# Optimization experiments

Measured on AMD Instinct MI355X. Metric: run time of the kernel, lower is better.

## Reference

```python
import jax, jax.numpy as jnp
import numpy as np

D_MODEL, D_INNER, D_STATE, DT_RANK, D_CONV = 768, 1536, 16, 48, 4
B, L = 2, 2048


def setup_inputs() -> dict:
    key = jax.random.key(0)
    ks = jax.random.split(key, 8)
    s = 0.02
    return {
        "x": jax.random.normal(ks[0], (B, L, D_MODEL), jnp.float32),
        "norm_w": jnp.ones((D_MODEL,), jnp.float32),
        "in_proj_w": jax.random.normal(ks[1], (2 * D_INNER, D_MODEL), jnp.float32) * s,
        "conv_w": jax.random.normal(ks[2], (D_INNER, 1, D_CONV), jnp.float32) * s,
        "conv_b": jnp.zeros((D_INNER,), jnp.float32),
        "x_proj_w": jax.random.normal(ks[3], (DT_RANK + 2 * D_STATE, D_INNER), jnp.float32) * s,
        "dt_proj_w": jax.random.normal(ks[4], (D_INNER, DT_RANK), jnp.float32) * s,
        "dt_proj_b": jax.random.normal(ks[5], (D_INNER,), jnp.float32) * s,
        "A_log": jnp.broadcast_to(jnp.log(jnp.arange(1, D_STATE + 1, dtype=jnp.float32)), (D_INNER, D_STATE)).copy(),
        "D": jnp.ones((D_INNER,), jnp.float32),
        "out_proj_w": jax.random.normal(ks[6], (D_MODEL, D_INNER), jnp.float32) * s,
    }


def _mamba_block(x, norm_w, in_proj_w, conv_w, conv_b, x_proj_w,
                 dt_proj_w, dt_proj_b, A_log, D, out_proj_w):
    residual = x
    # RMSNorm
    h = x * jax.lax.rsqrt(jnp.mean(x * x, axis=-1, keepdims=True) + 1e-5) * norm_w
    # in_proj -> chunk into (hs, gate)
    xz = jnp.einsum('bld,ed->ble', h, in_proj_w)          # [B,L,2*Di]
    xh, z = jnp.split(xz, 2, axis=-1)                     # each [B,L,Di]
    # causal depthwise conv1d (kernel D_CONV) + SiLU
    xt = jnp.transpose(xh, (0, 2, 1))                     # [B,Di,L]
    xt = jnp.pad(xt, ((0, 0), (0, 0), (D_CONV - 1, 0)))
    xc = jax.lax.conv_general_dilated(xt, conv_w, (1,), 'VALID',
                                      feature_group_count=D_INNER)
    xc = jax.nn.silu(xc + conv_b[None, :, None])
    xc = jnp.transpose(xc, (0, 2, 1))                     # [B,L,Di]
    # x_proj -> (dt, B, C)
    proj = jnp.einsum('bld,ed->ble', xc, x_proj_w)        # [B,L,dt_rank+2N]
    dt, Bm, Cm = jnp.split(proj, [DT_RANK, DT_RANK + D_STATE], axis=-1)
    delta = jax.nn.softplus(jnp.einsum('blr,dr->bld', dt, dt_proj_w) + dt_proj_b)  # [B,L,Di]
    A = -jnp.exp(A_log)                                   # [Di,N]
    dA = jnp.exp(delta[..., None] * A)                    # [B,L,Di,N]
    dBx = delta[..., None] * Bm[:, :, None, :] * xc[..., None]  # [B,L,Di,N]
    # selective scan over the sequence axis
    def step(hst, inp):
        dA_t, dBx_t, C_t = inp                            # [B,Di,N],[B,Di,N],[B,N]
        hst = dA_t * hst + dBx_t
        y = jnp.einsum('bdn,bn->bd', hst, C_t)
        return hst, y
    h0 = jnp.zeros((x.shape[0], D_INNER, D_STATE), x.dtype)
    _, ys = jax.lax.scan(step, h0, (jnp.moveaxis(dA, 1, 0),
                                    jnp.moveaxis(dBx, 1, 0),
                                    jnp.moveaxis(Cm, 1, 0)))
    y = jnp.moveaxis(ys, 0, 1)                            # [B,L,Di]
    y = y + xc * D                                        # skip connection D
    y = y * jax.nn.silu(z)                                # gate
    out = jnp.einsum('bld,ed->ble', y, out_proj_w)        # [B,L,Dm]
    return residual + out, residual


def reference(x, norm_w, in_proj_w, conv_w, conv_b, x_proj_w,
              dt_proj_w, dt_proj_b, A_log, D, out_proj_w):
    return _mamba_block(x, norm_w, in_proj_w, conv_w, conv_b, x_proj_w,
                        dt_proj_w, dt_proj_b, A_log, D, out_proj_w)
```

## Files before the change

### kernel.cpp

```cpp
#include <hip/hip_runtime.h>
#include <cstdint>
#include <cstddef>

typedef __bf16 bf16_t;
typedef __bf16 bf16x8 __attribute__((ext_vector_type(8)));
typedef float  f32x4  __attribute__((ext_vector_type(4)));

#define D_MODEL 768
#define D_INNER 1536
#define D_STATE 16
#define DT_RANK 48
#define NB      2
#define SEQ     2048
#define NTOK    (NB*SEQ)
#define XPROJ_N (DT_RANK + 2*D_STATE)
#define LC      32
#define NCHUNK  (SEQ/LC)
#define XP_KS   4
#define XP_KC   (D_INNER/XP_KS)

#define N_INW (2*D_INNER*D_MODEL)
#define N_XPW (XPROJ_N*D_INNER)
#define N_DTW (D_INNER*DT_RANK)
#define N_OPW (D_MODEL*D_INNER)
#define N_CVT (N_INW+N_XPW+N_DTW+N_OPW)
#define CVT_BLOCKS (N_CVT/1024)

typedef __attribute__((address_space(1))) void gvoid_t;
typedef __attribute__((address_space(3))) void lvoid_t;
__device__ __forceinline__ void g2lds16(const bf16_t* g, bf16_t* l) {
    __builtin_amdgcn_global_load_lds((gvoid_t*)g, (lvoid_t*)l, 16, 0, 0);
}

__global__ __launch_bounds__(256)
void prep_kernel(const float* __restrict__ in_proj_w, bf16_t* __restrict__ w_in,
                 const float* __restrict__ x_proj_w,  bf16_t* __restrict__ w_xp,
                 const float* __restrict__ dt_proj_w, bf16_t* __restrict__ w_dt,
                 const float* __restrict__ out_proj_w,bf16_t* __restrict__ w_op,
                 const float* __restrict__ x, const float* __restrict__ norm_w,
                 bf16_t* __restrict__ h, float* __restrict__ proj,
                 float* __restrict__ out0, float* __restrict__ out1) {
    const int blk = blockIdx.x;
    const int tid = threadIdx.x;
    if (blk < CVT_BLOCKS) {
        int off = (blk * 256 + tid) * 4;
        const float* s; bf16_t* d;
        if (off < N_INW) { s = in_proj_w + off; d = w_in + off; }
        else if ((off -= N_INW) < N_XPW) { s = x_proj_w + off; d = w_xp + off; }
        else if ((off -= N_XPW) < N_DTW) { s = dt_proj_w + off; d = w_dt + off; }
        else { off -= N_DTW; s = out_proj_w + off; d = w_op + off; }
        float4 v = *(const float4*)s;
        d[0] = (bf16_t)v.x; d[1] = (bf16_t)v.y;
        d[2] = (bf16_t)v.z; d[3] = (bf16_t)v.w;
        return;
    }
    int t = blk - CVT_BLOCKS;
    if (tid < XPROJ_N) proj[(size_t)t * XPROJ_N + tid] = 0.f;
    const float* xr = x + (size_t)t * D_MODEL;
    float v[3];
    float ss = 0.f;
#pragma unroll
    for (int i = 0; i < 3; i++) { v[i] = xr[tid + 256*i]; ss += v[i]*v[i]; }
#pragma unroll
    for (int off = 32; off >= 1; off >>= 1) ss += __shfl_down(ss, off);
    __shared__ float red[4];
    int lane = tid & 63, wv = tid >> 6;
    if (lane == 0) red[wv] = ss;
    __syncthreads();
    float tot = red[0] + red[1] + red[2] + red[3];
    float r = rsqrtf(tot * (1.f/(float)D_MODEL) + 1e-5f);
#pragma unroll
    for (int i = 0; i < 3; i++) {
        size_t idx = (size_t)t*D_MODEL + tid + 256*i;
        h[idx] = (bf16_t)(v[i] * r * norm_w[tid + 256*i]);
        out0[idx] = v[i];
        out1[idx] = v[i];
    }
}

__global__ __launch_bounds__(256)
void gemm_nt128(const bf16_t* __restrict__ A, int lda,
                const bf16_t* __restrict__ B, int ldb,
                bf16_t* __restrict__ C, int ldc, int K) {
    __shared__ __align__(16) bf16_t As[2][128*32];
    __shared__ __align__(16) bf16_t Bs[2][128*32];
    const int tid = threadIdx.x;
    const int wave = tid >> 6, lane = tid & 63;
    const int quad = lane >> 4, l16 = lane & 15;
    const int nbx = gridDim.x, nby = gridDim.y;
    int bid = blockIdx.y * nbx + blockIdx.x;
    const int cpx = (nbx * nby) >> 3;
    bid = (bid & 7) * cpx + (bid >> 3);
    const int m0 = (bid / nby) * 128, n0 = (bid % nby) * 128;
    const int wr = (wave >> 1) * 64, wc = (wave & 1) * 64;

    const int s0 = tid, s1 = tid + 256;
    const int r0 = s0 >> 2, q0 = ((s0 & 3) ^ ((r0 >> 1) & 3)) << 3;
    const int r1 = s1 >> 2, q1 = ((s1 & 3) ^ ((r1 >> 1) & 3)) << 3;

    const bf16_t* Ar0 = A + (size_t)(m0 + r0)*lda + q0;
    const bf16_t* Ar1 = A + (size_t)(m0 + r1)*lda + q1;
    const bf16_t* Br0 = B + (size_t)(n0 + r0)*ldb + q0;
    const bf16_t* Br1 = B + (size_t)(n0 + r1)*ldb + q1;

    f32x4 acc[4][4] = {};
    const int nit = K >> 5;

    g2lds16(Ar0, &As[0][wave*512]);
    g2lds16(Ar1, &As[0][wave*512 + 2048]);
    g2lds16(Br0, &Bs[0][wave*512]);
    g2lds16(Br1, &Bs[0][wave*512 + 2048]);

    for (int it = 0; it < nit; it++) {
        __syncthreads();
        if (it + 1 < nit) {
            int k = (it + 1) << 5;
            int nb = (it + 1) & 1;
            g2lds16(Ar0 + k, &As[nb][wave*512]);
            g2lds16(Ar1 + k, &As[nb][wave*512 + 2048]);
            g2lds16(Br0 + k, &Bs[nb][wave*512]);
            g2lds16(Br1 + k, &Bs[nb][wave*512 + 2048]);
        }
        const int buf = it & 1;
        bf16x8 af[4], bfr[4];
#pragma unroll
        for (int i = 0; i < 4; i++) {
            int rr = wr + i*16 + l16;
            af[i] = *(const bf16x8*)&As[buf][rr*32 + ((quad ^ ((rr >> 1) & 3)) << 3)];
        }
#pragma unroll
        for (int j = 0; j < 4; j++) {
            int rr = wc + j*16 + l16;
            bfr[j] = *(const bf16x8*)&Bs[buf][rr*32 + ((quad ^ ((rr >> 1) & 3)) << 3)];
        }
#pragma unroll
        for (int i = 0; i < 4; i++)
#pragma unroll
            for (int j = 0; j < 4; j++)
                acc[i][j] = __builtin_amdgcn_mfma_f32_16x16x32_bf16(af[i], bfr[j], acc[i][j], 0, 0, 0);
    }

#pragma unroll
    for (int i = 0; i < 4; i++)
#pragma unroll
        for (int j = 0; j < 4; j++) {
            int n = n0 + wc + j*16 + l16;
#pragma unroll
            for (int rr = 0; rr < 4; rr++) {
                int m = m0 + wr + i*16 + quad*4 + rr;
                C[(size_t)m * ldc + n] = (bf16_t)acc[i][j][rr];
            }
        }
}

__global__ __launch_bounds__(256)
void gemm_op(const bf16_t* __restrict__ A, const bf16_t* __restrict__ B,
             float* __restrict__ C) {
    __shared__ __align__(16) bf16_t As[2][128*32];
    __shared__ __align__(16) bf16_t Bs[2][128*32];
    const int tid = threadIdx.x;
    const int wave = tid >> 6, lane = tid & 63;
    const int quad = lane >> 4, l16 = lane & 15;
    const int nbx = gridDim.x, nby = gridDim.y;
    int bid = blockIdx.y * nbx + blockIdx.x;
    const int cpx = (nbx * nby) >> 3;
    bid = (bid & 7) * cpx + (bid >> 3);
    const int m0 = (bid / nby) * 128, n0 = (bid % nby) * 128;
    const int kbase = blockIdx.z * (D_INNER/2);
    const int wr = (wave >> 1) * 64, wc = (wave & 1) * 64;

    const int s0 = tid, s1 = tid + 256;
    const int r0 = s0 >> 2, q0 = ((s0 & 3) ^ ((r0 >> 1) & 3)) << 3;
    const int r1 = s1 >> 2, q1 = ((s1 & 3) ^ ((r1 >> 1) & 3)) << 3;

    const bf16_t* Ar0 = A + (size_t)(m0 + r0)*D_INNER + kbase + q0;
    const bf16_t* Ar1 = A + (size_t)(m0 + r1)*D_INNER + kbase + q1;
    const bf16_t* Br0 = B + (size_t)(n0 + r0)*D_INNER + kbase + q0;
    const bf16_t* Br1 = B + (size_t)(n0 + r1)*D_INNER + kbase + q1;

    f32x4 acc[4][4] = {};
    const int nit = (D_INNER/2) >> 5;

    g2lds16(Ar0, &As[0][wave*512]);
    g2lds16(Ar1, &As[0][wave*512 + 2048]);
    g2lds16(Br0, &Bs[0][wave*512]);
    g2lds16(Br1, &Bs[0][wave*512 + 2048]);

    for (int it = 0; it < nit; it++) {
        __syncthreads();
        if (it + 1 < nit) {
            int k = (it + 1) << 5;
            int nb = (it + 1) & 1;
            g2lds16(Ar0 + k, &As[nb][wave*512]);
            g2lds16(Ar1 + k, &As[nb][wave*512 + 2048]);
            g2lds16(Br0 + k, &Bs[nb][wave*512]);
            g2lds16(Br1 + k, &Bs[nb][wave*512 + 2048]);
        }
        const int buf = it & 1;
        bf16x8 af[4], bfr[4];
#pragma unroll
        for (int i = 0; i < 4; i++) {
            int rr = wr + i*16 + l16;
            af[i] = *(const bf16x8*)&As[buf][rr*32 + ((quad ^ ((rr >> 1) & 3)) << 3)];
        }
#pragma unroll
        for (int j = 0; j < 4; j++) {
            int rr = wc + j*16 + l16;
            bfr[j] = *(const bf16x8*)&Bs[buf][rr*32 + ((quad ^ ((rr >> 1) & 3)) << 3)];
        }
#pragma unroll
        for (int i = 0; i < 4; i++)
#pragma unroll
            for (int j = 0; j < 4; j++)
                acc[i][j] = __builtin_amdgcn_mfma_f32_16x16x32_bf16(af[i], bfr[j], acc[i][j], 0, 0, 0);
    }

#pragma unroll
    for (int i = 0; i < 4; i++)
#pragma unroll
        for (int j = 0; j < 4; j++) {
            int n = n0 + wc + j*16 + l16;
#pragma unroll
            for (int rr = 0; rr < 4; rr++) {
                int m = m0 + wr + i*16 + quad*4 + rr;
                unsafeAtomicAdd(&C[(size_t)m * D_MODEL + n], acc[i][j][rr]);
            }
        }
}

__global__ __launch_bounds__(256)
void gemm_xp(const bf16_t* __restrict__ A, const bf16_t* __restrict__ B,
             float* __restrict__ proj) {
    __shared__ __align__(16) bf16_t As[64*32];
    __shared__ __align__(16) bf16_t Bs[64*32];
    const int tid = threadIdx.x;
    const int m0 = blockIdx.x * 64, n0 = blockIdx.y * 64, kbase = blockIdx.z * XP_KC;
    const int r  = tid >> 2, p8 = (tid & 3) << 3;
    const int q8 = (((tid & 3) ^ ((r >> 1) & 3)) << 3);
    const int wave = tid >> 6, lane = tid & 63;
    const int quad = lane >> 4, l16 = lane & 15;

    f32x4 acc[4] = {{0.f,0.f,0.f,0.f},{0.f,0.f,0.f,0.f},
                    {0.f,0.f,0.f,0.f},{0.f,0.f,0.f,0.f}};

    for (int k0 = 0; k0 < XP_KC; k0 += 32) {
        int gk = kbase + k0 + q8;
        uint4 va = *(const uint4*)(A + (size_t)(m0 + r) * D_INNER + gk);
        *(uint4*)&As[r*32 + p8] = va;
        uint4 vb = {0u,0u,0u,0u};
        int nr = n0 + r;
        if (nr < XPROJ_N)
            vb = *(const uint4*)(B + (size_t)nr * D_INNER + gk);
        *(uint4*)&Bs[r*32 + p8] = vb;

        __syncthreads();
        int ra = wave*16 + l16;
        bf16x8 af = *(const bf16x8*)&As[ra*32 + ((quad ^ ((ra >> 1) & 3)) << 3)];
#pragma unroll
        for (int nt = 0; nt < 4; nt++) {
            int rb = nt*16 + l16;
            bf16x8 bfg = *(const bf16x8*)&Bs[rb*32 + ((quad ^ ((rb >> 1) & 3)) << 3)];
            acc[nt] = __builtin_amdgcn_mfma_f32_16x16x32_bf16(af, bfg, acc[nt], 0, 0, 0);
        }
        __syncthreads();
    }

#pragma unroll
    for (int nt = 0; nt < 4; nt++) {
        int n = n0 + nt*16 + l16;
        if (n >= XPROJ_N) continue;
#pragma unroll
        for (int rr = 0; rr < 4; rr++) {
            int m = m0 + wave*16 + quad*4 + rr;
            unsafeAtomicAdd(&proj[(size_t)m * XPROJ_N + n], acc[nt][rr]);
        }
    }
}

__global__ __launch_bounds__(192)
void conv_silu_kernel(const bf16_t* __restrict__ xz,
                      const float* __restrict__ cw,
                      const float* __restrict__ cb,
                      bf16_t* __restrict__ xc) {
    const int t0 = blockIdx.x * 8;
    const int l0 = t0 & (SEQ - 1);
    const int d = threadIdx.x * 8;

    float cwf[32];
#pragma unroll
    for (int q = 0; q < 8; q++)
        *(float4*)&cwf[q*4] = *(const float4*)&cw[d*4 + q*4];

    float cbv[8];
    *(float4*)&cbv[0] = *(const float4*)&cb[d];
    *(float4*)&cbv[4] = *(const float4*)&cb[d+4];

    bf16x8 rows[11];
#pragma unroll
    for (int r = 0; r < 11; r++) {
        if (l0 - 3 + r >= 0) {
            rows[r] = *(const bf16x8*)&xz[(size_t)(t0 - 3 + r) * (2*D_INNER) + d];
        } else {
#pragma unroll
            for (int i = 0; i < 8; i++) rows[r][i] = (bf16_t)0.f;
        }
    }

#pragma unroll
    for (int tt = 0; tt < 8; tt++) {
        float acc[8];
#pragma unroll
        for (int i = 0; i < 8; i++) acc[i] = cbv[i];
#pragma unroll
        for (int k = 0; k < 4; k++)
#pragma unroll
            for (int i = 0; i < 8; i++)
                acc[i] += (float)rows[tt + k][i] * cwf[i*4 + k];
        bf16x8 o;
#pragma unroll
        for (int i = 0; i < 8; i++) {
            float s = acc[i] / (1.f + __expf(-acc[i]));
            o[i] = (bf16_t)s;
        }
        *(bf16x8*)&xc[(size_t)(t0 + tt) * D_INNER + d] = o;
    }
}

__device__ __forceinline__ void delta_mfma32(
    const float* __restrict__ proj, const bf16_t* __restrict__ w_dt,
    const float* __restrict__ bias, int bx, size_t tbase, int tid,
    bf16_t* As , bf16_t* Bs , bf16_t* Ds ) {
    const int wave = tid >> 6, lane = tid & 63;
    const int quad = lane >> 4, l16 = lane & 15;
    const int r  = tid >> 2;
    const int p8 = (tid & 3) << 3;
    const int x3 = ((tid & 3) ^ ((r >> 1) & 3)) << 3;

    f32x4 acc[2][4] = {};

#pragma unroll
    for (int kc = 0; kc < 2; kc++) {
        const int k0 = kc * 32;
        if (r < 32) {
            int gk = k0 + x3;
            bf16x8 v;
            if (gk < DT_RANK) {
                const float* src = proj + (tbase + r) * XPROJ_N + gk;
                float4 f0 = *(const float4*)src;
                float4 f1 = *(const float4*)(src + 4);
                v[0]=(bf16_t)f0.x; v[1]=(bf16_t)f0.y; v[2]=(bf16_t)f0.z; v[3]=(bf16_t)f0.w;
                v[4]=(bf16_t)f1.x; v[5]=(bf16_t)f1.y; v[6]=(bf16_t)f1.z; v[7]=(bf16_t)f1.w;
            } else {
#pragma unroll
                for (int i = 0; i < 8; i++) v[i] = (bf16_t)0.f;
            }
            *(bf16x8*)&As[r*32 + p8] = v;
        }
#pragma unroll
        for (int it = 0; it < 4; it++) {
            int row = r + 64*it;
            uint4 vb = {0u,0u,0u,0u};
            if (k0 + x3 < DT_RANK)
                vb = *(const uint4*)(w_dt + (size_t)(bx*256 + row)*DT_RANK + k0 + x3);
            *(uint4*)&Bs[row*32 + p8] = vb;
        }
        __syncthreads();
        bf16x8 af[2];
#pragma unroll
        for (int mi = 0; mi < 2; mi++) {
            int rr = mi*16 + l16;
            af[mi] = *(const bf16x8*)&As[rr*32 + ((quad ^ ((rr >> 1) & 3)) << 3)];
        }
#pragma unroll
        for (int nj = 0; nj < 4; nj++) {
            int rb = wave*64 + nj*16 + l16;
            bf16x8 bfr = *(const bf16x8*)&Bs[rb*32 + ((quad ^ ((rb >> 1) & 3)) << 3)];
#pragma unroll
            for (int mi = 0; mi < 2; mi++)
                acc[mi][nj] = __builtin_amdgcn_mfma_f32_16x16x32_bf16(af[mi], bfr, acc[mi][nj], 0, 0, 0);
        }
        __syncthreads();
    }
#pragma unroll
    for (int nj = 0; nj < 4; nj++) {
        int dloc = wave*64 + nj*16 + l16;
        float b = bias[bx*256 + dloc];
#pragma unroll
        for (int mi = 0; mi < 2; mi++) {
#pragma unroll
            for (int rr2 = 0; rr2 < 4; rr2++) {
                int t = mi*16 + quad*4 + rr2;
                float u = acc[mi][nj][rr2] + b;
                float sp = (u > 20.f) ? u : log1pf(__expf(u));
                Ds[t*256 + dloc] = (bf16_t)sp;
            }
        }
    }
    __syncthreads();
}

__global__ __launch_bounds__(256)
void scan_part1(const bf16_t* __restrict__ xc,
                const float* __restrict__ proj,
                const bf16_t* __restrict__ w_dt,
                const float* __restrict__ dt_bias,
                const float* __restrict__ A_log,
                float* __restrict__ chunk_h, float* __restrict__ chunk_P) {
    __shared__ __align__(16) bf16_t uraw[32*32 + 256*32];
    bf16_t* As = uraw;
    bf16_t* Bs = uraw + 32*32;
    bf16_t* Ds = uraw;
    __shared__ float Bsv[LC][D_STATE];
    const int tid = threadIdx.x;
    const int bx = blockIdx.x;
    const int c = blockIdx.y, b = blockIdx.z;
    const size_t tbase = (size_t)b*SEQ + (size_t)c*LC;
    for (int i = tid; i < LC*D_STATE; i += 256) {
        int l = i >> 4, n = i & 15;
        Bsv[l][n] = proj[(tbase + l)*XPROJ_N + DT_RANK + n];
    }
    delta_mfma32(proj, w_dt, dt_bias, bx, tbase, tid, As, Bs, Ds);

    const int d = bx*256 + tid;
    float Av2[D_STATE];
#pragma unroll
    for (int n = 0; n < D_STATE; n++)
        Av2[n] = -__expf(A_log[d*D_STATE + n]) * 1.44269504f;
    float s[D_STATE];
#pragma unroll
    for (int n = 0; n < D_STATE; n++) s[n] = 0.f;
    float sdv = 0.f;
    for (int g = 0; g < LC/8; g++) {
        float dvv[8], xv[8];
#pragma unroll
        for (int j = 0; j < 8; j++) {
            int l = g*8 + j;
            dvv[j] = (float)Ds[l*256 + tid];
            xv[j]  = (float)xc[(tbase + l)*D_INNER + d];
        }
#pragma unroll
        for (int j = 0; j < 8; j++) {
            int l = g*8 + j;
            float dv = dvv[j];
            float dx = dv * xv[j];
            sdv += dv;
#pragma unroll
            for (int n = 0; n < D_STATE; n++) {
                float a = __builtin_amdgcn_exp2f(dv * Av2[n]);
                s[n] = a * s[n] + dx * Bsv[l][n];
            }
        }
    }
    size_t base = (((size_t)b*NCHUNK + c)*D_INNER + d)*D_STATE;
#pragma unroll
    for (int n = 0; n < D_STATE; n++) {
        chunk_h[base + n] = s[n];
        chunk_P[base + n] = __builtin_amdgcn_exp2f(Av2[n] * sdv);
    }
}

__global__ __launch_bounds__(256)
void scan_part2(float* __restrict__ chunk_h, const float* __restrict__ chunk_P) {
    int gid = blockIdx.x * 256 + threadIdx.x;
    int b  = gid / (D_INNER * D_STATE);
    int dn = gid - b * (D_INNER * D_STATE);
    const size_t cs = (size_t)D_INNER * D_STATE;
    size_t base = (size_t)b * NCHUNK * cs + dn;
    float H = 0.f;
    float S[8], P[8];
#pragma unroll
    for (int j = 0; j < 8; j++) {
        S[j] = chunk_h[base + (size_t)j * cs];
        P[j] = chunk_P[base + (size_t)j * cs];
    }
    for (int g = 0; g < NCHUNK/8; g++) {
        float S2[8], P2[8];
        if (g < NCHUNK/8 - 1) {
#pragma unroll
            for (int j = 0; j < 8; j++) {
                S2[j] = chunk_h[base + (size_t)((g+1)*8 + j) * cs];
                P2[j] = chunk_P[base + (size_t)((g+1)*8 + j) * cs];
            }
        }
#pragma unroll
        for (int j = 0; j < 8; j++) {
            size_t idx = base + (size_t)(g*8 + j) * cs;
            chunk_h[idx] = H;
            H = fmaf(P[j], H, S[j]);
        }
#pragma unroll
        for (int j = 0; j < 8; j++) { S[j] = S2[j]; P[j] = P2[j]; }
    }
}

__global__ __launch_bounds__(256)
void scan_part3(const bf16_t* __restrict__ xc,
                const float* __restrict__ proj,
                const bf16_t* __restrict__ w_dt,
                const float* __restrict__ dt_bias,
                const bf16_t* __restrict__ xz,
                const float* __restrict__ A_log,
                const float* __restrict__ Dw,
                const float* __restrict__ chunk_h,
                bf16_t* __restrict__ y) {
    __shared__ __align__(16) bf16_t uraw[32*32 + 256*32];
    bf16_t* As = uraw;
    bf16_t* Bs = uraw + 32*32;
    bf16_t* Ds = uraw;
    __shared__ float Bsv[LC][D_STATE];
    __shared__ float Csv[LC][D_STATE];
    const int tid = threadIdx.x;
    const int bx = blockIdx.x;
    const int c = blockIdx.y, b = blockIdx.z;
    const size_t tbase = (size_t)b*SEQ + (size_t)c*LC;
    for (int i = tid; i < LC*D_STATE; i += 256) {
        int l = i >> 4, n = i & 15;
        Bsv[l][n] = proj[(tbase + l)*XPROJ_N + DT_RANK + n];
        Csv[l][n] = proj[(tbase + l)*XPROJ_N + DT_RANK + D_STATE + n];
    }
    delta_mfma32(proj, w_dt, dt_bias, bx, tbase, tid, As, Bs, Ds);

    const int d = bx*256 + tid;
    float Av2[D_STATE];
#pragma unroll
    for (int n = 0; n < D_STATE; n++)
        Av2[n] = -__expf(A_log[d*D_STATE + n]) * 1.44269504f;
    const float Dv = Dw[d];
    float s[D_STATE];
    size_t base = (((size_t)b*NCHUNK + c)*D_INNER + d)*D_STATE;
#pragma unroll
    for (int n = 0; n < D_STATE; n++) s[n] = chunk_h[base + n];
    for (int g = 0; g < LC/8; g++) {
        float dvv[8], xv[8], zv[8];
#pragma unroll
        for (int j = 0; j < 8; j++) {
            int l = g*8 + j;
            size_t t = tbase + l;
            dvv[j] = (float)Ds[l*256 + tid];
            xv[j]  = (float)xc[t*D_INNER + d];
            zv[j]  = (float)xz[t*(2*D_INNER) + D_INNER + d];
        }
#pragma unroll
        for (int j = 0; j < 8; j++) {
            int l = g*8 + j;
            float dv = dvv[j];
            float xcv = xv[j];
            float dx = dv * xcv;
            float acc = 0.f;
#pragma unroll
            for (int n = 0; n < D_STATE; n++) {
                float a = __builtin_amdgcn_exp2f(dv * Av2[n]);
                s[n] = a * s[n] + dx * Bsv[l][n];
                acc += s[n] * Csv[l][n];
            }
            float zf = zv[j];
            float gt = zf / (1.f + __expf(-zf));
            y[(tbase + l)*D_INNER + d] = (bf16_t)((acc + xcv * Dv) * gt);
        }
    }
}

extern "C" void kernel_launch(void* const* d_in, const int* in_sizes, int n_in,
                              void* d_out, int out_size, void* d_ws, size_t ws_size,
                              hipStream_t stream) {
    const float* x          = (const float*)d_in[0];
    const float* norm_w     = (const float*)d_in[1];
    const float* in_proj_w  = (const float*)d_in[2];
    const float* conv_w     = (const float*)d_in[3];
    const float* conv_b     = (const float*)d_in[4];
    const float* x_proj_w   = (const float*)d_in[5];
    const float* dt_proj_w  = (const float*)d_in[6];
    const float* dt_proj_b  = (const float*)d_in[7];
    const float* A_log      = (const float*)d_in[8];
    const float* Dw         = (const float*)d_in[9];
    const float* out_proj_w = (const float*)d_in[10];

    float* out0 = (float*)d_out;
    float* out1 = out0 + (size_t)NTOK * D_MODEL;

    const size_t n_chunkst = (size_t)NB*NCHUNK*D_INNER*D_STATE;

    char* ws = (char*)d_ws;
    bf16_t* w_in  = (bf16_t*)ws;  ws += (size_t)N_INW * sizeof(bf16_t);
    bf16_t* w_xp  = (bf16_t*)ws;  ws += (size_t)N_XPW * sizeof(bf16_t);
    bf16_t* w_dt  = (bf16_t*)ws;  ws += (size_t)N_DTW * sizeof(bf16_t);
    bf16_t* w_op  = (bf16_t*)ws;  ws += (size_t)N_OPW * sizeof(bf16_t);
    bf16_t* h     = (bf16_t*)ws;  ws += (size_t)NTOK * D_MODEL   * sizeof(bf16_t);
    bf16_t* xz    = (bf16_t*)ws;  ws += (size_t)NTOK * 2*D_INNER * sizeof(bf16_t);
    bf16_t* xc    = (bf16_t*)ws;  ws += (size_t)NTOK * D_INNER   * sizeof(bf16_t);
    bf16_t* y     = (bf16_t*)ws;  ws += (size_t)NTOK * D_INNER   * sizeof(bf16_t);
    float*  proj  = (float*)ws;   ws += (size_t)NTOK * XPROJ_N   * sizeof(float);
    float*  ch    = (float*)ws;   ws += n_chunkst * sizeof(float);
    float*  cP    = (float*)ws;   ws += n_chunkst * sizeof(float);

    prep_kernel<<<CVT_BLOCKS + NTOK, 256, 0, stream>>>(
        in_proj_w, w_in, x_proj_w, w_xp, dt_proj_w, w_dt, out_proj_w, w_op,
        x, norm_w, h, proj, out0, out1);
    gemm_nt128<<<dim3(NTOK/128, (2*D_INNER)/128), 256, 0, stream>>>(
        h, D_MODEL, w_in, D_MODEL, xz, 2*D_INNER, D_MODEL);
    conv_silu_kernel<<<NTOK/8, 192, 0, stream>>>(xz, conv_w, conv_b, xc);
    gemm_xp<<<dim3(NTOK/64, 2, XP_KS), 256, 0, stream>>>(xc, w_xp, proj);
    scan_part1<<<dim3(D_INNER/256, NCHUNK, NB), 256, 0, stream>>>(
        xc, proj, w_dt, dt_proj_b, A_log, ch, cP);
    scan_part2<<<(int)((size_t)NB*D_INNER*D_STATE/256), 256, 0, stream>>>(ch, cP);
    scan_part3<<<dim3(D_INNER/256, NCHUNK, NB), 256, 0, stream>>>(
        xc, proj, w_dt, dt_proj_b, xz, A_log, Dw, ch, y);
    gemm_op<<<dim3(NTOK/128, D_MODEL/128, 2), 256, 0, stream>>>(y, w_op, out0);
}
```

Measured before the change: 294.3 us.

## Split scan state dimension across thread pairs, 128 channels per block

The chunked scan kernels now assign two threads per channel, each owning 8 of the 16 state entries. Blocks cover 128 channels instead of 256, which doubles the grid. The delta MFMA helper is shrunk to match, and B/C are read from shared memory as float4 vectors. The two partial C·h dot products are combined with a lane shuffle, trading duplicated delta/x/z loads and exp work per pair for more parallelism and fewer registers per thread.

```diff
diff --git a/kernel.cpp b/kernel.cpp
--- a/kernel.cpp
+++ b/kernel.cpp
@@ -326,7 +326,7 @@
     }
 }
 
-__device__ __forceinline__ void delta_mfma32(
+__device__ __forceinline__ void delta_mfma128(
     const float* __restrict__ proj, const bf16_t* __restrict__ w_dt,
     const float* __restrict__ bias, int bx, size_t tbase, int tid,
     bf16_t* As , bf16_t* Bs , bf16_t* Ds ) {
@@ -336,7 +336,7 @@
     const int p8 = (tid & 3) << 3;
     const int x3 = ((tid & 3) ^ ((r >> 1) & 3)) << 3;
 
-    f32x4 acc[2][4] = {};
+    f32x4 acc[2][2] = {};
 
 #pragma unroll
     for (int kc = 0; kc < 2; kc++) {
@@ -357,11 +357,11 @@
             *(bf16x8*)&As[r*32 + p8] = v;
         }
 #pragma unroll
-        for (int it = 0; it < 4; it++) {
+        for (int it = 0; it < 2; it++) {
             int row = r + 64*it;
             uint4 vb = {0u,0u,0u,0u};
             if (k0 + x3 < DT_RANK)
-                vb = *(const uint4*)(w_dt + (size_t)(bx*256 + row)*DT_RANK + k0 + x3);
+                vb = *(const uint4*)(w_dt + (size_t)(bx*128 + row)*DT_RANK + k0 + x3);
             *(uint4*)&Bs[row*32 + p8] = vb;
         }
         __syncthreads();
@@ -372,8 +372,8 @@
             af[mi] = *(const bf16x8*)&As[rr*32 + ((quad ^ ((rr >> 1) & 3)) << 3)];
         }
 #pragma unroll
-        for (int nj = 0; nj < 4; nj++) {
-            int rb = wave*64 + nj*16 + l16;
+        for (int nj = 0; nj < 2; nj++) {
+            int rb = wave*32 + nj*16 + l16;
             bf16x8 bfr = *(const bf16x8*)&Bs[rb*32 + ((quad ^ ((rb >> 1) & 3)) << 3)];
 #pragma unroll
             for (int mi = 0; mi < 2; mi++)
@@ -382,9 +382,9 @@
         __syncthreads();
     }
 #pragma unroll
-    for (int nj = 0; nj < 4; nj++) {
-        int dloc = wave*64 + nj*16 + l16;
-        float b = bias[bx*256 + dloc];
+    for (int nj = 0; nj < 2; nj++) {
+        int dloc = wave*32 + nj*16 + l16;
+        float b = bias[bx*128 + dloc];
 #pragma unroll
         for (int mi = 0; mi < 2; mi++) {
 #pragma unroll
@@ -392,7 +392,7 @@
                 int t = mi*16 + quad*4 + rr2;
                 float u = acc[mi][nj][rr2] + b;
                 float sp = (u > 20.f) ? u : log1pf(__expf(u));
-                Ds[t*256 + dloc] = (bf16_t)sp;
+                Ds[t*128 + dloc] = (bf16_t)sp;
             }
         }
     }
@@ -406,11 +406,11 @@
                 const float* __restrict__ dt_bias,
                 const float* __restrict__ A_log,
                 float* __restrict__ chunk_h, float* __restrict__ chunk_P) {
-    __shared__ __align__(16) bf16_t uraw[32*32 + 256*32];
+    __shared__ __align__(16) bf16_t uraw[32*32 + 128*32];
     bf16_t* As = uraw;
     bf16_t* Bs = uraw + 32*32;
     bf16_t* Ds = uraw;
-    __shared__ float Bsv[LC][D_STATE];
+    __shared__ __align__(16) float Bsv[LC][D_STATE];
     const int tid = threadIdx.x;
     const int bx = blockIdx.x;
     const int c = blockIdx.y, b = blockIdx.z;
@@ -419,23 +419,26 @@
         int l = i >> 4, n = i & 15;
         Bsv[l][n] = proj[(tbase + l)*XPROJ_N + DT_RANK + n];
     }
-    delta_mfma32(proj, w_dt, dt_bias, bx, tbase, tid, As, Bs, Ds);
-
-    const int d = bx*256 + tid;
-    float Av2[D_STATE];
-#pragma unroll
-    for (int n = 0; n < D_STATE; n++)
-        Av2[n] = -__expf(A_log[d*D_STATE + n]) * 1.44269504f;
-    float s[D_STATE];
-#pragma unroll
-    for (int n = 0; n < D_STATE; n++) s[n] = 0.f;
+    delta_mfma128(proj, w_dt, dt_bias, bx, tbase, tid, As, Bs, Ds);
+
+    const int ch  = tid >> 1;
+    const int hf  = tid & 1;
+    const int d   = bx*128 + ch;
+    const int n0s = hf*8;
+    float Av2[8];
+#pragma unroll
+    for (int n = 0; n < 8; n++)
+        Av2[n] = -__expf(A_log[d*D_STATE + n0s + n]) * 1.44269504f;
+    float s[8];
+#pragma unroll
+    for (int n = 0; n < 8; n++) s[n] = 0.f;
     float sdv = 0.f;
     for (int g = 0; g < LC/8; g++) {
         float dvv[8], xv[8];
 #pragma unroll
         for (int j = 0; j < 8; j++) {
             int l = g*8 + j;
-            dvv[j] = (float)Ds[l*256 + tid];
+            dvv[j] = (float)Ds[l*128 + ch];
             xv[j]  = (float)xc[(tbase + l)*D_INNER + d];
         }
 #pragma unroll
@@ -444,16 +447,23 @@
             float dv = dvv[j];
             float dx = dv * xv[j];
             sdv += dv;
-#pragma unroll
-            for (int n = 0; n < D_STATE; n++) {
+            f32x4 B0 = *(const f32x4*)&Bsv[l][n0s];
+            f32x4 B1 = *(const f32x4*)&Bsv[l][n0s + 4];
+#pragma unroll
+            for (int n = 0; n < 4; n++) {
                 float a = __builtin_amdgcn_exp2f(dv * Av2[n]);
-                s[n] = a * s[n] + dx * Bsv[l][n];
-            }
-        }
-    }
-    size_t base = (((size_t)b*NCHUNK + c)*D_INNER + d)*D_STATE;
-#pragma unroll
-    for (int n = 0; n < D_STATE; n++) {
+                s[n] = a * s[n] + dx * B0[n];
+            }
+#pragma unroll
+            for (int n = 0; n < 4; n++) {
+                float a = __builtin_amdgcn_exp2f(dv * Av2[4+n]);
+                s[4+n] = a * s[4+n] + dx * B1[n];
+            }
+        }
+    }
+    size_t base = (((size_t)b*NCHUNK + c)*D_INNER + d)*D_STATE + n0s;
+#pragma unroll
+    for (int n = 0; n < 8; n++) {
         chunk_h[base + n] = s[n];
         chunk_P[base + n] = __builtin_amdgcn_exp2f(Av2[n] * sdv);
     }
@@ -503,12 +513,12 @@
                 const float* __restrict__ Dw,
                 const float* __restrict__ chunk_h,
                 bf16_t* __restrict__ y) {
-    __shared__ __align__(16) bf16_t uraw[32*32 + 256*32];
+    __shared__ __align__(16) bf16_t uraw[32*32 + 128*32];
     bf16_t* As = uraw;
     bf16_t* Bs = uraw + 32*32;
     bf16_t* Ds = uraw;
-    __shared__ float Bsv[LC][D_STATE];
-    __shared__ float Csv[LC][D_STATE];
+    __shared__ __align__(16) float Bsv[LC][D_STATE];
+    __shared__ __align__(16) float Csv[LC][D_STATE];
     const int tid = threadIdx.x;
     const int bx = blockIdx.x;
     const int c = blockIdx.y, b = blockIdx.z;
@@ -518,25 +528,28 @@
         Bsv[l][n] = proj[(tbase + l)*XPROJ_N + DT_RANK + n];
         Csv[l][n] = proj[(tbase + l)*XPROJ_N + DT_RANK + D_STATE + n];
     }
-    delta_mfma32(proj, w_dt, dt_bias, bx, tbase, tid, As, Bs, Ds);
-
-    const int d = bx*256 + tid;
-    float Av2[D_STATE];
-#pragma unroll
-    for (int n = 0; n < D_STATE; n++)
-        Av2[n] = -__expf(A_log[d*D_STATE + n]) * 1.44269504f;
+    delta_mfma128(proj, w_dt, dt_bias, bx, tbase, tid, As, Bs, Ds);
+
+    const int ch  = tid >> 1;
+    const int hf  = tid & 1;
+    const int d   = bx*128 + ch;
+    const int n0s = hf*8;
+    float Av2[8];
+#pragma unroll
+    for (int n = 0; n < 8; n++)
+        Av2[n] = -__expf(A_log[d*D_STATE + n0s + n]) * 1.44269504f;
     const float Dv = Dw[d];
-    float s[D_STATE];
-    size_t base = (((size_t)b*NCHUNK + c)*D_INNER + d)*D_STATE;
-#pragma unroll
-    for (int n = 0; n < D_STATE; n++) s[n] = chunk_h[base + n];
+    float s[8];
+    size_t base = (((size_t)b*NCHUNK + c)*D_INNER + d)*D_STATE + n0s;
+#pragma unroll
+    for (int n = 0; n < 8; n++) s[n] = chunk_h[base + n];
     for (int g = 0; g < LC/8; g++) {
         float dvv[8], xv[8], zv[8];
 #pragma unroll
         for (int j = 0; j < 8; j++) {
             int l = g*8 + j;
             size_t t = tbase + l;
-            dvv[j] = (float)Ds[l*256 + tid];
+            dvv[j] = (float)Ds[l*128 + ch];
             xv[j]  = (float)xc[t*D_INNER + d];
             zv[j]  = (float)xz[t*(2*D_INNER) + D_INNER + d];
         }
@@ -547,15 +560,28 @@
             float xcv = xv[j];
             float dx = dv * xcv;
             float acc = 0.f;
-#pragma unroll
-            for (int n = 0; n < D_STATE; n++) {
+            f32x4 B0 = *(const f32x4*)&Bsv[l][n0s];
+            f32x4 B1 = *(const f32x4*)&Bsv[l][n0s + 4];
+            f32x4 C0 = *(const f32x4*)&Csv[l][n0s];
+            f32x4 C1 = *(const f32x4*)&Csv[l][n0s + 4];
+#pragma unroll
+            for (int n = 0; n < 4; n++) {
                 float a = __builtin_amdgcn_exp2f(dv * Av2[n]);
-                s[n] = a * s[n] + dx * Bsv[l][n];
-                acc += s[n] * Csv[l][n];
-            }
-            float zf = zv[j];
-            float gt = zf / (1.f + __expf(-zf));
-            y[(tbase + l)*D_INNER + d] = (bf16_t)((acc + xcv * Dv) * gt);
+                s[n] = a * s[n] + dx * B0[n];
+                acc += s[n] * C0[n];
+            }
+#pragma unroll
+            for (int n = 0; n < 4; n++) {
+                float a = __builtin_amdgcn_exp2f(dv * Av2[4+n]);
+                s[4+n] = a * s[4+n] + dx * B1[n];
+                acc += s[4+n] * C1[n];
+            }
+            float tot = acc + __shfl_xor(acc, 1);
+            if (hf == 0) {
+                float zf = zv[j];
+                float gt = zf / (1.f + __expf(-zf));
+                y[(tbase + l)*D_INNER + d] = (bf16_t)((tot + xcv * Dv) * gt);
+            }
         }
     }
 }
@@ -600,10 +626,10 @@
         h, D_MODEL, w_in, D_MODEL, xz, 2*D_INNER, D_MODEL);
     conv_silu_kernel<<<NTOK/8, 192, 0, stream>>>(xz, conv_w, conv_b, xc);
     gemm_xp<<<dim3(NTOK/64, 2, XP_KS), 256, 0, stream>>>(xc, w_xp, proj);
-    scan_part1<<<dim3(D_INNER/256, NCHUNK, NB), 256, 0, stream>>>(
+    scan_part1<<<dim3(D_INNER/128, NCHUNK, NB), 256, 0, stream>>>(
         xc, proj, w_dt, dt_proj_b, A_log, ch, cP);
     scan_part2<<<(int)((size_t)NB*D_INNER*D_STATE/256), 256, 0, stream>>>(ch, cP);
-    scan_part3<<<dim3(D_INNER/256, NCHUNK, NB), 256, 0, stream>>>(
+    scan_part3<<<dim3(D_INNER/128, NCHUNK, NB), 256, 0, stream>>>(
         xc, proj, w_dt, dt_proj_b, xz, A_log, Dw, ch, y);
     gemm_op<<<dim3(NTOK/128, D_MODEL/128, 2), 256, 0, stream>>>(y, w_op, out0);
 }
```

Result: faster. 281.2 us (-4.4%).
